# Performance work log

Measured on AMD Instinct MI355X. Metric: run time of the kernel, lower is better.

The kernel has to match this reference:

```python
import jax, jax.numpy as jnp
import numpy as np

TOPK_FRAC = 0.9
LEAKY_SLOPE = 0.01
BN_EPS = 1e-5


def setup_inputs() -> dict:
    key = jax.random.key(0)
    k1, k2 = jax.random.split(key)
    B, C_in, N, C_out = 8, 256, 2048, 256
    x = jax.random.normal(k1, (B, C_in, N), dtype=jnp.float32)
    stdv = 1.0 / np.sqrt(C_out)
    weight = jax.random.uniform(k2, (C_in, C_out), dtype=jnp.float32, minval=-stdv, maxval=stdv)
    bn_weight = jnp.zeros((C_out,), dtype=jnp.float32)
    bn_bias = jnp.zeros((C_out,), dtype=jnp.float32)
    return {"x": x, "weight": weight, "bn_weight": bn_weight, "bn_bias": bn_bias}


def _norm_adj(xn):
    # xn: [B, N, C]
    adj = jax.nn.softmax(jnp.einsum('bnc,bmc->bnm', xn, xn), axis=-1)  # [B,N,N]
    N = adj.shape[1]
    k = int(round(N * TOPK_FRAC))
    topv, _ = jax.lax.top_k(adj, k)                     # [B,N,k]
    thresh = topv[..., -1:]                              # k-th largest per row
    return jnp.where(adj >= thresh, adj, 0.0)           # keep top-k, zero rest


def reference(x, weight, bn_weight, bn_bias):
    # x: [B, C_in, N] -> [B, N, C_in]
    xn = jnp.transpose(x, (0, 2, 1))
    adj = _norm_adj(xn)                                  # [B,N,N]
    support = jnp.einsum('bnc,cd->bnd', xn, weight)      # [B,N,C_out]
    out = jnp.einsum('bnm,bmd->bnd', adj, support)       # [B,N,C_out]
    out = jnp.transpose(out, (0, 2, 1))                  # [B,C_out,N]
    out = jnp.where(out >= 0, out, LEAKY_SLOPE * out)    # LeakyReLU
    # BatchNorm1d (training-mode batch stats) over (B, N) per channel
    mean = jnp.mean(out, axis=(0, 2), keepdims=True)
    var = jnp.mean(jnp.square(out - mean), axis=(0, 2), keepdims=True)
    out = (out - mean) * jax.lax.rsqrt(var + BN_EPS)
    return out * bn_weight[None, :, None] + bn_bias[None, :, None]
```

## Files before the change

### kernel.cpp

```cpp
#include <hip/hip_runtime.h>

#define B_ 8
#define C_ 256
#define N_ 2048
#define D_ 256
#define KKEEP 1843
#define LEAKY 0.01f
#define EPS 1e-5f

using short8  = __attribute__((ext_vector_type(8))) short;
using ushort8 = __attribute__((ext_vector_type(8))) unsigned short;
using ushort4v = __attribute__((ext_vector_type(4))) unsigned short;
using f32x4   = __attribute__((ext_vector_type(4))) float;

__device__ inline unsigned short f2bf(float x) {
  unsigned u = __float_as_uint(x);
  u += 0x7fffu + ((u >> 16) & 1u);
  return (unsigned short)(u >> 16);
}
__device__ inline float bf2f(unsigned short u) { return __uint_as_float(((unsigned)u) << 16); }

__global__ __launch_bounds__(256) void k_transpose_cast(const float* __restrict__ src,
                                                        unsigned short* __restrict__ dst,
                                                        int rows, int cols,
                                                        size_t srcBatch, size_t dstBatch) {
  __shared__ float tile[32][33];
  int b = blockIdx.z;
  src += (size_t)b * srcBatch;
  dst += (size_t)b * dstBatch;
  int i0 = blockIdx.y * 32;
  int j0 = blockIdx.x * 32;
  int t = threadIdx.x;
  int tc = t & 31, tr = t >> 5;
#pragma unroll
  for (int k = 0; k < 4; ++k)
    tile[tr + k * 8][tc] = src[(size_t)(i0 + tr + k * 8) * cols + j0 + tc];
  __syncthreads();
  int r2 = t >> 3, q = t & 7;
  ushort4v v;
#pragma unroll
  for (int l = 0; l < 4; ++l) v[l] = f2bf(tile[q * 4 + l][r2]);
  *(ushort4v*)&dst[(size_t)(j0 + r2) * rows + i0 + q * 4] = v;
}

template<int K_, int BN, bool SWZ>
__global__ __launch_bounds__(256) void k_gemm(const short* __restrict__ A,
                                              const short* __restrict__ Bt,
                                              unsigned short* __restrict__ Cout,
                                              size_t aStride, size_t bStride, size_t cStride,
                                              int ldc, int nx) {
  constexpr int FI = (BN == 128) ? 4 : 2;
  __shared__ short As[128][44];
  __shared__ short Bs[BN][44];
  int b, bxi, byi;
  if constexpr (SWZ) {
    int lin = blockIdx.x;
    b = lin & 7;
    int rest = lin >> 3;
    bxi = rest % nx;
    byi = rest / nx;
  } else {
    b = blockIdx.z; bxi = blockIdx.x; byi = blockIdx.y;
  }
  A += (size_t)b * aStride;
  Bt += (size_t)b * bStride;
  int bi = byi * 128;
  int bj = bxi * BN;
  int t = threadIdx.x;
  int lane = t & 63, wid = t >> 6;
  int wr, wc;
  if constexpr (BN == 128) { wr = (wid >> 1) * 64; wc = (wid & 1) * 64; }
  else                     { wr = wid * 32;        wc = 0; }

  int r0 = t >> 2, k0 = (t & 3) * 8;
  int r1 = r0 + 64;
  const short* aP0 = A + (size_t)(bi + r0) * K_ + k0;
  const short* aP1 = A + (size_t)(bi + r1) * K_ + k0;
  const short* bP0 = Bt + (size_t)(bj + r0) * K_ + k0;
  const short* bP1 = Bt + (size_t)(bj + (BN == 128 ? r1 : r0)) * K_ + k0;

  short8 a0 = *(const short8*)aP0;
  short8 a1 = *(const short8*)aP1;
  short8 b0 = *(const short8*)bP0;
  short8 b1;
  if constexpr (BN == 128) b1 = *(const short8*)bP1;

  f32x4 acc[FI][4];
  f32x4 z = {0.f, 0.f, 0.f, 0.f};
#pragma unroll
  for (int i = 0; i < FI; ++i)
#pragma unroll
    for (int j = 0; j < 4; ++j) acc[i][j] = z;

  int fr = lane & 15;
  int ks = (lane >> 4) * 8;

  for (int c0 = 0; c0 < K_; c0 += 32) {
    __syncthreads();
    *(short8*)&As[r0][k0] = a0;
    *(short8*)&As[r1][k0] = a1;
    *(short8*)&Bs[r0][k0] = b0;
    if constexpr (BN == 128) *(short8*)&Bs[r1][k0] = b1;
    __syncthreads();
    if (c0 + 32 < K_) {
      a0 = *(const short8*)(aP0 + c0 + 32);
      a1 = *(const short8*)(aP1 + c0 + 32);
      b0 = *(const short8*)(bP0 + c0 + 32);
      if constexpr (BN == 128) b1 = *(const short8*)(bP1 + c0 + 32);
    }
    short8 af[FI], bf[4];
#pragma unroll
    for (int f = 0; f < FI; ++f) af[f] = *(const short8*)&As[wr + f * 16 + fr][ks];
#pragma unroll
    for (int f = 0; f < 4; ++f)  bf[f] = *(const short8*)&Bs[wc + f * 16 + fr][ks];
#pragma unroll
    for (int fi = 0; fi < FI; ++fi)
#pragma unroll
      for (int fj = 0; fj < 4; ++fj)
        acc[fi][fj] = __builtin_amdgcn_mfma_f32_16x16x32_bf16(af[fi], bf[fj], acc[fi][fj], 0, 0, 0);
  }

  int orow = (lane >> 4) * 4;
  int ocol = lane & 15;
#pragma unroll
  for (int fi = 0; fi < FI; ++fi)
#pragma unroll
    for (int fj = 0; fj < 4; ++fj)
#pragma unroll
      for (int r = 0; r < 4; ++r) {
        size_t idx = (size_t)b * cStride +
                     (size_t)(bi + wr + fi * 16 + orow + r) * ldc +
                     (size_t)(bj + wc + fj * 16 + ocol);
        Cout[idx] = f2bf(acc[fi][fj][r]);
      }
}

__global__ __launch_bounds__(256) void k_softmax_topk(unsigned short* __restrict__ S) {
  int t = threadIdx.x;
  int lane = t & 63, wv = t >> 6;
  size_t row = (size_t)blockIdx.x * 4 + wv;
  unsigned short* sr = S + row * N_;

  float e[32];
#pragma unroll
  for (int i = 0; i < 4; ++i) {
    ushort8 raw = *(const ushort8*)(sr + ((size_t)(i * 64 + lane)) * 8);
#pragma unroll
    for (int j = 0; j < 8; ++j) e[i * 8 + j] = bf2f(raw[j]);
  }

  float lm = e[0];
#pragma unroll
  for (int j = 1; j < 32; ++j) lm = fmaxf(lm, e[j]);
#pragma unroll
  for (int m = 1; m <= 16; m <<= 1) lm = fmaxf(lm, __shfl_xor(lm, m));
  lm = fmaxf(__shfl(lm, 0), __shfl(lm, 32));

  float ls = 0.f;
#pragma unroll
  for (int j = 0; j < 32; ++j) { e[j] = __expf(e[j] - lm); ls += e[j]; }
#pragma unroll
  for (int m = 1; m <= 16; m <<= 1) ls += __shfl_xor(ls, m);
  ls = __shfl(ls, 0) + __shfl(ls, 32);
  float inv = 1.0f / ls;

  unsigned kp[16], vo[16];
#pragma unroll
  for (int q = 0; q < 16; ++q)
    kp[q] = (unsigned)f2bf(e[q]) | ((unsigned)f2bf(e[q + 16]) << 16);
#pragma unroll
  for (int q = 0; q < 16; ++q)
    vo[q] = (unsigned)f2bf(e[2 * q] * inv) | ((unsigned)f2bf(e[2 * q + 1] * inv) << 16);

  unsigned tp[16];
#pragma unroll
  for (int q = 0; q < 16; ++q) tp[q] = kp[q];
#pragma unroll
  for (int sI = 0; sI < 4; ++sI) {
    const int s = 8 >> sI;
    const unsigned msk = (s == 8) ? 0x00FF00FFu : (s == 4) ? 0x0F0F0F0Fu
                       : (s == 2) ? 0x33333333u : 0x55555555u;
#pragma unroll
    for (int k = 0; k < 16; ++k) {
      if ((k & s) == 0) {
        unsigned tt = ((tp[k] >> s) ^ tp[k + s]) & msk;
        tp[k + s] ^= tt;
        tp[k]     ^= tt << s;
      }
    }
  }

  unsigned alive = 0xFFFFFFFFu, prefix = 0u;
  int need = KKEEP;
#pragma unroll
  for (int b = 12; b >= 0; b -= 2) {
    unsigned p1 = tp[b + 1], p0 = tp[b];
    unsigned hi = alive & p1;
    unsigned m3 = hi & p0, m2 = hi & ~p0, m1v = (alive & ~p1) & p0;
    unsigned packed = (unsigned)__popc(m3) | ((unsigned)__popc(m2) << 11) |
                      ((unsigned)__popc(m1v) << 22);
#pragma unroll
    for (int m = 1; m <= 16; m <<= 1) packed += __shfl_xor(packed, m);
    unsigned v0 = __shfl(packed, 0), v32 = __shfl(packed, 32);
    int C3 = (int)((v0 & 0x7FFu) + (v32 & 0x7FFu));
    int C2 = (int)(((v0 >> 11) & 0x7FFu) + ((v32 >> 11) & 0x7FFu));
    int C1 = (int)(((v0 >> 22) & 0x7FFu) + ((v32 >> 22) & 0x7FFu));
    int cum2 = C3 + C2, cum1 = cum2 + C1;
    if (C3 >= need)        { alive = m3;  prefix |= 3u << b; }
    else if (cum2 >= need) { alive = m2;  prefix |= 2u << b; need -= C3; }
    else if (cum1 >= need) { alive = m1v; prefix |= 1u << b; need -= cum2; }
    else                   { alive ^= (m3 | m2 | m1v);       need -= cum1; }
  }

#pragma unroll
  for (int i = 0; i < 4; ++i) {
    ushort8 o;
#pragma unroll
    for (int j = 0; j < 8; ++j) {
      int idx = i * 8 + j;
      unsigned key = (kp[idx & 15] >> ((idx >> 4) * 16)) & 0xFFFFu;
      unsigned val = (vo[idx >> 1] >> ((idx & 1) * 16)) & 0xFFFFu;
      o[j] = (key >= prefix) ? (unsigned short)val : (unsigned short)0;
    }
    *(ushort8*)(sr + ((size_t)(i * 64 + lane)) * 8) = o;
  }
}

__global__ __launch_bounds__(256) void k_pv(const short* __restrict__ A,
                                            const short* __restrict__ Bt,
                                            unsigned short* __restrict__ pre,
                                            float* __restrict__ ps, float* __restrict__ pss) {
  __shared__ short As[128][68];
  __shared__ short Bs[64][68];
  int lin = blockIdx.x;
  int b = lin & 7;
  int rest = lin >> 3;
  int bxi = rest & 3;
  int byi = rest >> 2;
  const short* Ab = A + (size_t)b * N_ * N_;
  const short* Bb = Bt + (size_t)b * D_ * N_;
  int bi = byi * 128, bj = bxi * 64;
  int t = threadIdx.x, lane = t & 63, wid = t >> 6;
  int wr = wid * 32;

  int r = t >> 3, c8 = (t & 7) * 8;
  const short* aP0 = Ab + (size_t)(bi + r) * N_ + c8;
  const short* aP1 = Ab + (size_t)(bi + r + 32) * N_ + c8;
  const short* aP2 = Ab + (size_t)(bi + r + 64) * N_ + c8;
  const short* aP3 = Ab + (size_t)(bi + r + 96) * N_ + c8;
  const short* bP0 = Bb + (size_t)(bj + r) * N_ + c8;
  const short* bP1 = Bb + (size_t)(bj + r + 32) * N_ + c8;

  short8 a0 = *(const short8*)aP0;
  short8 a1 = *(const short8*)aP1;
  short8 a2 = *(const short8*)aP2;
  short8 a3 = *(const short8*)aP3;
  short8 b0 = *(const short8*)bP0;
  short8 b1 = *(const short8*)bP1;

  f32x4 acc[2][4];
  f32x4 z = {0.f, 0.f, 0.f, 0.f};
#pragma unroll
  for (int i = 0; i < 2; ++i)
#pragma unroll
    for (int j = 0; j < 4; ++j) acc[i][j] = z;

  int fr = lane & 15;
  int ks = (lane >> 4) * 8;

  for (int c0 = 0; c0 < N_; c0 += 64) {
    __syncthreads();
    *(short8*)&As[r][c8] = a0;
    *(short8*)&As[r + 32][c8] = a1;
    *(short8*)&As[r + 64][c8] = a2;
    *(short8*)&As[r + 96][c8] = a3;
    *(short8*)&Bs[r][c8] = b0;
    *(short8*)&Bs[r + 32][c8] = b1;
    __syncthreads();
    if (c0 + 64 < N_) {
      a0 = *(const short8*)(aP0 + c0 + 64);
      a1 = *(const short8*)(aP1 + c0 + 64);
      a2 = *(const short8*)(aP2 + c0 + 64);
      a3 = *(const short8*)(aP3 + c0 + 64);
      b0 = *(const short8*)(bP0 + c0 + 64);
      b1 = *(const short8*)(bP1 + c0 + 64);
    }
#pragma unroll
    for (int ksub = 0; ksub < 2; ++ksub) {
      short8 af[2], bf[4];
#pragma unroll
      for (int f = 0; f < 2; ++f) af[f] = *(const short8*)&As[wr + f * 16 + fr][ksub * 32 + ks];
#pragma unroll
      for (int f = 0; f < 4; ++f) bf[f] = *(const short8*)&Bs[f * 16 + fr][ksub * 32 + ks];
#pragma unroll
      for (int fi = 0; fi < 2; ++fi)
#pragma unroll
        for (int fj = 0; fj < 4; ++fj)
          acc[fi][fj] = __builtin_amdgcn_mfma_f32_16x16x32_bf16(af[fi], bf[fj], acc[fi][fj], 0, 0, 0);
    }
  }

  int orow = (lane >> 4) * 4;
  int ocol = lane & 15;
  float s4[4] = {0.f, 0.f, 0.f, 0.f}, ss4[4] = {0.f, 0.f, 0.f, 0.f};
#pragma unroll
  for (int fi = 0; fi < 2; ++fi)
#pragma unroll
    for (int rr = 0; rr < 4; ++rr) {
      int rowg = bi + wr + fi * 16 + orow + rr;
      size_t base = ((size_t)b * N_ + rowg) * D_ + bj;
#pragma unroll
      for (int fj = 0; fj < 4; ++fj) {
        float v = acc[fi][fj][rr];
        v = (v >= 0.f) ? v : LEAKY * v;
        pre[base + fj * 16 + ocol] = f2bf(v);
        s4[fj] += v;
        ss4[fj] = fmaf(v, v, ss4[fj]);
      }
    }
#pragma unroll
  for (int fj = 0; fj < 4; ++fj) {
    s4[fj] += __shfl_xor(s4[fj], 16);  s4[fj] += __shfl_xor(s4[fj], 32);
    ss4[fj] += __shfl_xor(ss4[fj], 16); ss4[fj] += __shfl_xor(ss4[fj], 32);
  }
  __syncthreads();
  float* sred = (float*)As;
  if (lane < 16) {
#pragma unroll
    for (int fj = 0; fj < 4; ++fj) {
      sred[(wid * 4 + fj) * 16 + lane] = s4[fj];
      sred[256 + (wid * 4 + fj) * 16 + lane] = ss4[fj];
    }
  }
  __syncthreads();
  if (t < 64) {
    float s = 0.f, ss = 0.f;
#pragma unroll
    for (int w4 = 0; w4 < 4; ++w4) {
      s  += sred[(w4 * 4 + (t >> 4)) * 16 + (t & 15)];
      ss += sred[256 + (w4 * 4 + (t >> 4)) * 16 + (t & 15)];
    }
    ps[(size_t)lin * 64 + t] = s;
    pss[(size_t)lin * 64 + t] = ss;
  }
}

__global__ void k_final(const float* __restrict__ ps, const float* __restrict__ pss,
                        const float* __restrict__ bnw, const float* __restrict__ bnb,
                        float* __restrict__ scale, float* __restrict__ shift) {
  int t = threadIdx.x;
  int bxi = t >> 6, col = t & 63;
  float s = 0.f, ss = 0.f;
  for (int byi = 0; byi < 16; ++byi)
    for (int bb = 0; bb < 8; ++bb) {
      int lin = (byi * 4 + bxi) * 8 + bb;
      s += ps[(size_t)lin * 64 + col];
      ss += pss[(size_t)lin * 64 + col];
    }
  const float invN = 1.0f / (B_ * N_);
  float mean = s * invN;
  float var = fmaf(-mean, mean, ss * invN);
  float istd = rsqrtf(var + EPS);
  float sc = istd * bnw[t];
  scale[t] = sc;
  shift[t] = fmaf(-mean, sc, bnb[t]);
}

__global__ __launch_bounds__(256) void k_out(const unsigned short* __restrict__ pre,
                                             const float* __restrict__ scale,
                                             const float* __restrict__ shift,
                                             float* __restrict__ out) {
  __shared__ float tile[32][33];
  int blk = blockIdx.x;
  int d0 = (blk % (D_ / 32)) * 32;
  int n0 = ((blk / (D_ / 32)) % (N_ / 32)) * 32;
  int b = blk / ((D_ / 32) * (N_ / 32));
  int tc = threadIdx.x & 31;
  int tr = threadIdx.x >> 5;
  const unsigned short* pb = pre + ((size_t)b * N_ + n0) * D_ + d0;
#pragma unroll
  for (int i = 0; i < 4; ++i) {
    int r = tr + i * 8;
    tile[r][tc] = bf2f(pb[(size_t)r * D_ + tc]);
  }
  __syncthreads();
  float* ob = out + ((size_t)b * D_ + d0) * N_ + n0;
#pragma unroll
  for (int i = 0; i < 4; ++i) {
    int r = tr + i * 8;
    float vv = tile[tc][r];
    ob[(size_t)r * N_ + tc] = fmaf(vv, scale[d0 + r], shift[d0 + r]);
  }
}

extern "C" void kernel_launch(void* const* d_in, const int* in_sizes, int n_in,
                              void* d_out, int out_size, void* d_ws, size_t ws_size,
                              hipStream_t stream) {
  const float* x = (const float*)d_in[0];
  const float* W = (const float*)d_in[1];
  const float* bnw = (const float*)d_in[2];
  const float* bnb = (const float*)d_in[3];
  float* out = (float*)d_out;

  char* w = (char*)d_ws;
  short* xt = (short*)w;            w += (size_t)B_ * N_ * C_ * 2;
  short* wt = (short*)w;            w += (size_t)D_ * C_ * 2;
  short* supT = (short*)w;          w += (size_t)B_ * D_ * N_ * 2;
  short* S = (short*)w;             w += (size_t)B_ * N_ * N_ * 2;
  unsigned short* pre = (unsigned short*)w; w += (size_t)B_ * N_ * D_ * 2;
  float* ps = (float*)w;            w += (size_t)512 * 64 * 4;
  float* pss = (float*)w;           w += (size_t)512 * 64 * 4;
  float* scale = (float*)w;         w += D_ * 4;
  float* shift = (float*)w;         w += D_ * 4;

  k_transpose_cast<<<dim3(N_ / 32, C_ / 32, B_), 256, 0, stream>>>(
      x, (unsigned short*)xt, C_, N_, (size_t)C_ * N_, (size_t)N_ * C_);
  k_transpose_cast<<<dim3(D_ / 32, C_ / 32, 1), 256, 0, stream>>>(
      W, (unsigned short*)wt, C_, D_, 0, 0);

  k_gemm<C_, 64, false><<<dim3(N_ / 64, 2, B_), 256, 0, stream>>>(
      wt, xt, (unsigned short*)supT, 0, (size_t)N_ * C_, (size_t)D_ * N_, N_, 0);

  k_gemm<C_, 128, true><<<dim3(16 * 16 * B_, 1, 1), 256, 0, stream>>>(
      xt, xt, (unsigned short*)S, (size_t)N_ * C_, (size_t)N_ * C_, (size_t)N_ * N_, N_, 16);

  k_softmax_topk<<<B_ * N_ / 4, 256, 0, stream>>>((unsigned short*)S);

  k_pv<<<dim3(4 * 16 * B_, 1, 1), 256, 0, stream>>>(S, supT, pre, ps, pss);

  k_final<<<1, 256, 0, stream>>>(ps, pss, bnw, bnb, scale, shift);
  k_out<<<B_ * (N_ / 32) * (D_ / 32), 256, 0, stream>>>(pre, scale, shift, out);
}
```

Measured before the change: 120.7 us.

## Use direct global-to-LDS loads with XOR-swizzled tiles in GEMM kernels

Replaces the register-staged global loads in the GEMM and PV kernels with global_load_lds 16-byte direct-to-LDS loads. The LDS tiles become unpadded 64-wide rows with an XOR swizzle to avoid bank conflicts. K-step widens to 64, and the support GEMM now uses 128x128 tiles with a swizzled grid. This drops the register prefetch, so loads are no longer overlapped with the MFMA work of the previous step, which could expose memory latency.

New measurement: 108.4 us. 10.2% less time.

```diff
diff --git a/kernel.cpp b/kernel.cpp
--- a/kernel.cpp
+++ b/kernel.cpp
@@ -19,6 +19,12 @@
   return (unsigned short)(u >> 16);
 }
 __device__ inline float bf2f(unsigned short u) { return __uint_as_float(((unsigned)u) << 16); }
+
+__device__ inline void gload16(const void* g, void* l) {
+  __builtin_amdgcn_global_load_lds(
+      (const __attribute__((address_space(1))) void*)g,
+      (__attribute__((address_space(3))) void*)l, 16, 0, 0);
+}
 
 __global__ __launch_bounds__(256) void k_transpose_cast(const float* __restrict__ src,
                                                         unsigned short* __restrict__ dst,
@@ -43,87 +49,67 @@
   *(ushort4v*)&dst[(size_t)(j0 + r2) * rows + i0 + q * 4] = v;
 }
 
-template<int K_, int BN, bool SWZ>
+template<int K_, int NX>
 __global__ __launch_bounds__(256) void k_gemm(const short* __restrict__ A,
                                               const short* __restrict__ Bt,
                                               unsigned short* __restrict__ Cout,
                                               size_t aStride, size_t bStride, size_t cStride,
-                                              int ldc, int nx) {
-  constexpr int FI = (BN == 128) ? 4 : 2;
-  __shared__ short As[128][44];
-  __shared__ short Bs[BN][44];
-  int b, bxi, byi;
-  if constexpr (SWZ) {
-    int lin = blockIdx.x;
-    b = lin & 7;
-    int rest = lin >> 3;
-    bxi = rest % nx;
-    byi = rest / nx;
-  } else {
-    b = blockIdx.z; bxi = blockIdx.x; byi = blockIdx.y;
-  }
-  A += (size_t)b * aStride;
-  Bt += (size_t)b * bStride;
-  int bi = byi * 128;
-  int bj = bxi * BN;
-  int t = threadIdx.x;
-  int lane = t & 63, wid = t >> 6;
-  int wr, wc;
-  if constexpr (BN == 128) { wr = (wid >> 1) * 64; wc = (wid & 1) * 64; }
-  else                     { wr = wid * 32;        wc = 0; }
-
-  int r0 = t >> 2, k0 = (t & 3) * 8;
-  int r1 = r0 + 64;
-  const short* aP0 = A + (size_t)(bi + r0) * K_ + k0;
-  const short* aP1 = A + (size_t)(bi + r1) * K_ + k0;
-  const short* bP0 = Bt + (size_t)(bj + r0) * K_ + k0;
-  const short* bP1 = Bt + (size_t)(bj + (BN == 128 ? r1 : r0)) * K_ + k0;
-
-  short8 a0 = *(const short8*)aP0;
-  short8 a1 = *(const short8*)aP1;
-  short8 b0 = *(const short8*)bP0;
-  short8 b1;
-  if constexpr (BN == 128) b1 = *(const short8*)bP1;
-
-  f32x4 acc[FI][4];
+                                              int ldc) {
+  __shared__ short As[128][64];
+  __shared__ short Bs[128][64];
+  int lin = blockIdx.x;
+  int b = lin & 7;
+  int rest = lin >> 3;
+  int bxi = rest % NX, byi = rest / NX;
+  const short* Ab = A + (size_t)b * aStride;
+  const short* Bb = Bt + (size_t)b * bStride;
+  int bi = byi * 128, bj = bxi * 128;
+  int t = threadIdx.x, lane = t & 63, wid = t >> 6;
+  int wr = (wid >> 1) * 64, wc = (wid & 1) * 64;
+  int fr = lane & 15;
+  int wbase = wid * 512;
+
+  f32x4 acc[4][4];
   f32x4 z = {0.f, 0.f, 0.f, 0.f};
 #pragma unroll
-  for (int i = 0; i < FI; ++i)
+  for (int i = 0; i < 4; ++i)
 #pragma unroll
     for (int j = 0; j < 4; ++j) acc[i][j] = z;
 
-  int fr = lane & 15;
-  int ks = (lane >> 4) * 8;
-
-  for (int c0 = 0; c0 < K_; c0 += 32) {
+  for (int c0 = 0; c0 < K_; c0 += 64) {
+    if (c0) __syncthreads();
+#pragma unroll
+    for (int i = 0; i < 4; ++i) {
+      int li = i * 256 + t;
+      int row = li >> 3, ch = li & 7;
+      int sw = ((ch ^ (row & 7)) << 3);
+      gload16(Ab + (size_t)(bi + row) * K_ + c0 + sw, (short*)As + i * 2048 + wbase);
+      gload16(Bb + (size_t)(bj + row) * K_ + c0 + sw, (short*)Bs + i * 2048 + wbase);
+    }
     __syncthreads();
-    *(short8*)&As[r0][k0] = a0;
-    *(short8*)&As[r1][k0] = a1;
-    *(short8*)&Bs[r0][k0] = b0;
-    if constexpr (BN == 128) *(short8*)&Bs[r1][k0] = b1;
-    __syncthreads();
-    if (c0 + 32 < K_) {
-      a0 = *(const short8*)(aP0 + c0 + 32);
-      a1 = *(const short8*)(aP1 + c0 + 32);
-      b0 = *(const short8*)(bP0 + c0 + 32);
-      if constexpr (BN == 128) b1 = *(const short8*)(bP1 + c0 + 32);
-    }
-    short8 af[FI], bf[4];
-#pragma unroll
-    for (int f = 0; f < FI; ++f) af[f] = *(const short8*)&As[wr + f * 16 + fr][ks];
-#pragma unroll
-    for (int f = 0; f < 4; ++f)  bf[f] = *(const short8*)&Bs[wc + f * 16 + fr][ks];
-#pragma unroll
-    for (int fi = 0; fi < FI; ++fi)
-#pragma unroll
-      for (int fj = 0; fj < 4; ++fj)
-        acc[fi][fj] = __builtin_amdgcn_mfma_f32_16x16x32_bf16(af[fi], bf[fj], acc[fi][fj], 0, 0, 0);
+#pragma unroll
+    for (int ksub = 0; ksub < 2; ++ksub) {
+      int cA = ksub * 4 + (lane >> 4);
+      short8 af[4], bf[4];
+#pragma unroll
+      for (int f = 0; f < 4; ++f) {
+        int R = wr + f * 16 + fr;
+        af[f] = *(const short8*)&As[R][(cA ^ (R & 7)) << 3];
+        int Rb = wc + f * 16 + fr;
+        bf[f] = *(const short8*)&Bs[Rb][(cA ^ (Rb & 7)) << 3];
+      }
+#pragma unroll
+      for (int fi = 0; fi < 4; ++fi)
+#pragma unroll
+        for (int fj = 0; fj < 4; ++fj)
+          acc[fi][fj] = __builtin_amdgcn_mfma_f32_16x16x32_bf16(af[fi], bf[fj], acc[fi][fj], 0, 0, 0);
+    }
   }
 
   int orow = (lane >> 4) * 4;
   int ocol = lane & 15;
 #pragma unroll
-  for (int fi = 0; fi < FI; ++fi)
+  for (int fi = 0; fi < 4; ++fi)
 #pragma unroll
     for (int fj = 0; fj < 4; ++fj)
 #pragma unroll
@@ -230,8 +216,8 @@
                                             const short* __restrict__ Bt,
                                             unsigned short* __restrict__ pre,
                                             float* __restrict__ ps, float* __restrict__ pss) {
-  __shared__ short As[128][68];
-  __shared__ short Bs[64][68];
+  __shared__ short As[128][64];
+  __shared__ short Bs[64][64];
   int lin = blockIdx.x;
   int b = lin & 7;
   int rest = lin >> 3;
@@ -242,21 +228,8 @@
   int bi = byi * 128, bj = bxi * 64;
   int t = threadIdx.x, lane = t & 63, wid = t >> 6;
   int wr = wid * 32;
-
-  int r = t >> 3, c8 = (t & 7) * 8;
-  const short* aP0 = Ab + (size_t)(bi + r) * N_ + c8;
-  const short* aP1 = Ab + (size_t)(bi + r + 32) * N_ + c8;
-  const short* aP2 = Ab + (size_t)(bi + r + 64) * N_ + c8;
-  const short* aP3 = Ab + (size_t)(bi + r + 96) * N_ + c8;
-  const short* bP0 = Bb + (size_t)(bj + r) * N_ + c8;
-  const short* bP1 = Bb + (size_t)(bj + r + 32) * N_ + c8;
-
-  short8 a0 = *(const short8*)aP0;
-  short8 a1 = *(const short8*)aP1;
-  short8 a2 = *(const short8*)aP2;
-  short8 a3 = *(const short8*)aP3;
-  short8 b0 = *(const short8*)bP0;
-  short8 b1 = *(const short8*)bP1;
+  int fr = lane & 15;
+  int wbase = wid * 512;
 
   f32x4 acc[2][4];
   f32x4 z = {0.f, 0.f, 0.f, 0.f};
@@ -265,33 +238,32 @@
 #pragma unroll
     for (int j = 0; j < 4; ++j) acc[i][j] = z;
 
-  int fr = lane & 15;
-  int ks = (lane >> 4) * 8;
-
   for (int c0 = 0; c0 < N_; c0 += 64) {
+    if (c0) __syncthreads();
+#pragma unroll
+    for (int i = 0; i < 4; ++i) {
+      int li = i * 256 + t;
+      int row = li >> 3, ch = li & 7;
+      int sw = ((ch ^ (row & 7)) << 3);
+      gload16(Ab + (size_t)(bi + row) * N_ + c0 + sw, (short*)As + i * 2048 + wbase);
+      if (i < 2)
+        gload16(Bb + (size_t)(bj + row) * N_ + c0 + sw, (short*)Bs + i * 2048 + wbase);
+    }
     __syncthreads();
-    *(short8*)&As[r][c8] = a0;
-    *(short8*)&As[r + 32][c8] = a1;
-    *(short8*)&As[r + 64][c8] = a2;
-    *(short8*)&As[r + 96][c8] = a3;
-    *(short8*)&Bs[r][c8] = b0;
-    *(short8*)&Bs[r + 32][c8] = b1;
-    __syncthreads();
-    if (c0 + 64 < N_) {
-      a0 = *(const short8*)(aP0 + c0 + 64);
-      a1 = *(const short8*)(aP1 + c0 + 64);
-      a2 = *(const short8*)(aP2 + c0 + 64);
-      a3 = *(const short8*)(aP3 + c0 + 64);
-      b0 = *(const short8*)(bP0 + c0 + 64);
-      b1 = *(const short8*)(bP1 + c0 + 64);
-    }
 #pragma unroll
     for (int ksub = 0; ksub < 2; ++ksub) {
+      int cA = ksub * 4 + (lane >> 4);
       short8 af[2], bf[4];
 #pragma unroll
-      for (int f = 0; f < 2; ++f) af[f] = *(const short8*)&As[wr + f * 16 + fr][ksub * 32 + ks];
-#pragma unroll
-      for (int f = 0; f < 4; ++f) bf[f] = *(const short8*)&Bs[f * 16 + fr][ksub * 32 + ks];
+      for (int f = 0; f < 2; ++f) {
+        int R = wr + f * 16 + fr;
+        af[f] = *(const short8*)&As[R][(cA ^ (R & 7)) << 3];
+      }
+#pragma unroll
+      for (int f = 0; f < 4; ++f) {
+        int Rb = f * 16 + fr;
+        bf[f] = *(const short8*)&Bs[Rb][(cA ^ (Rb & 7)) << 3];
+      }
 #pragma unroll
       for (int fi = 0; fi < 2; ++fi)
 #pragma unroll
@@ -418,15 +390,15 @@
   k_transpose_cast<<<dim3(D_ / 32, C_ / 32, 1), 256, 0, stream>>>(
       W, (unsigned short*)wt, C_, D_, 0, 0);
 
-  k_gemm<C_, 64, false><<<dim3(N_ / 64, 2, B_), 256, 0, stream>>>(
-      wt, xt, (unsigned short*)supT, 0, (size_t)N_ * C_, (size_t)D_ * N_, N_, 0);
-
-  k_gemm<C_, 128, true><<<dim3(16 * 16 * B_, 1, 1), 256, 0, stream>>>(
-      xt, xt, (unsigned short*)S, (size_t)N_ * C_, (size_t)N_ * C_, (size_t)N_ * N_, N_, 16);
+  k_gemm<C_, 16><<<dim3(8 * 16 * 2, 1, 1), 256, 0, stream>>>(
+      wt, xt, (unsigned short*)supT, 0, (size_t)N_ * C_, (size_t)D_ * N_, N_);
+
+  k_gemm<C_, 16><<<dim3(8 * 16 * 16, 1, 1), 256, 0, stream>>>(
+      xt, xt, (unsigned short*)S, (size_t)N_ * C_, (size_t)N_ * C_, (size_t)N_ * N_, N_);
 
   k_softmax_topk<<<B_ * N_ / 4, 256, 0, stream>>>((unsigned short*)S);
 
-  k_pv<<<dim3(4 * 16 * B_, 1, 1), 256, 0, stream>>>(S, supT, pre, ps, pss);
+  k_pv<<<dim3(4 * 16 * 8, 1, 1), 256, 0, stream>>>(S, supT, pre, ps, pss);
 
   k_final<<<1, 256, 0, stream>>>(ps, pss, bnw, bnb, scale, shift);
   k_out<<<B_ * (N_ / 32) * (D_ / 32), 256, 0, stream>>>(pre, scale, shift, out);
```
